# Performance work log

Measured on AMD Instinct MI355X. Metric: run time of the kernel, lower is better.

## Reference

```python
import jax, jax.numpy as jnp
import numpy as np

D_EMB = 1024
D_HEAD = 64
B = 4
T = 4096


def setup_inputs() -> dict:
    key = jax.random.key(0)
    kx, kk, kq, kv = jax.random.split(key, 4)
    s = 1.0 / np.sqrt(D_EMB)  # torch Linear default init scale (uniform bound)
    x = jax.random.normal(kx, (B, T, D_EMB), dtype=jnp.float32)
    Wk = jax.random.uniform(kk, (D_HEAD, D_EMB), jnp.float32, -s, s)
    Wq = jax.random.uniform(kq, (D_HEAD, D_EMB), jnp.float32, -s, s)
    Wv = jax.random.uniform(kv, (D_HEAD, D_EMB), jnp.float32, -s, s)
    return {"x": x, "Wk": Wk, "Wq": Wq, "Wv": Wv}


def reference(x, Wk, Wq, Wv):
    # x: (B, T, d_emb); W*: (d_head, d_emb) -- torch Linear stores (out, in)
    k = jnp.einsum('bte,he->bth', x, Wk)
    q = jnp.einsum('bte,he->bth', x, Wq)
    v = jnp.einsum('bte,he->bth', x, Wv)
    scale = D_HEAD ** (-0.5)
    a = jnp.einsum('bth,bsh->bts', q, k) * scale  # (B, T, T)
    Tlen = x.shape[-2]
    causal = jnp.tril(jnp.ones((Tlen, Tlen), dtype=bool))
    a = jnp.where(causal, a, -jnp.inf)
    a = jax.nn.softmax(a, axis=-1)
    return jnp.einsum('bts,bsh->bth', a, v)  # (B, T, d_head)
```

## Files before the change

### kernel.cpp

```cpp
#include <hip/hip_runtime.h>
#include <hip/hip_bf16.h>

#define D_EMB 1024
#define T_LEN 4096
#define NTASK2 544

typedef short short8 __attribute__((ext_vector_type(8)));
typedef float f32x4 __attribute__((ext_vector_type(4)));
typedef float f32x16 __attribute__((ext_vector_type(16)));
typedef float float4v __attribute__((ext_vector_type(4)));

__device__ __forceinline__ unsigned short f32_to_bf16(float f) {
    union { float f; unsigned int u; } c; c.f = f;
    unsigned int u = c.u;
    return (unsigned short)((u + 0x7FFFu + ((u >> 16) & 1u)) >> 16);
}
__device__ __forceinline__ float bf16_to_f32(unsigned short v) {
    union { unsigned int u; float f; } c; c.u = ((unsigned int)v) << 16;
    return c.f;
}
__device__ __forceinline__ unsigned cvtpk_bf16(float a, float b) {
    unsigned r;
    asm("v_cvt_pk_bf16_f32 %0, %1, %2" : "=v"(r) : "v"(a), "v"(b));
    return r;
}
__device__ __forceinline__ float xhalf_add(float x) {
    return x + __shfl_xor(x, 32);
}
__device__ __forceinline__ void gl_lds16(const void* g, void* l) {
    __builtin_amdgcn_global_load_lds(
        (const __attribute__((address_space(1))) unsigned int*)(g),
        (__attribute__((address_space(3))) unsigned int*)(l), 16, 0, 0);
}

#define QSCALE (0.125f * 1.44269504f)

__global__ __launch_bounds__(256) void convert_w(const float* __restrict__ Wk,
                                                 const float* __restrict__ Wq,
                                                 const float* __restrict__ Wv,
                                                 unsigned short* __restrict__ Wb) {
    int e = (blockIdx.x * 256 + threadIdx.x) * 8;
    const float* src;
    if (e < 65536) src = Wk + e;
    else if (e < 131072) src = Wq + (e - 65536);
    else src = Wv + (e - 131072);
    float4v a0 = *(const float4v*)src;
    float4v a1 = *(const float4v*)(src + 4);
    short8 r;
    r[0] = (short)f32_to_bf16(a0[0]); r[1] = (short)f32_to_bf16(a0[1]);
    r[2] = (short)f32_to_bf16(a0[2]); r[3] = (short)f32_to_bf16(a0[3]);
    r[4] = (short)f32_to_bf16(a1[0]); r[5] = (short)f32_to_bf16(a1[1]);
    r[6] = (short)f32_to_bf16(a1[2]); r[7] = (short)f32_to_bf16(a1[3]);
    int row = e >> 10;
    int dst = e ^ ((row & 7) << 3);
    *(short8*)(Wb + dst) = r;
}

__global__ __launch_bounds__(512) void qkv_chunk(const float* __restrict__ x,
                                                 const unsigned short* __restrict__ Wb,
                                                 unsigned short* __restrict__ Cp) {
    __shared__ __attribute__((aligned(16))) unsigned short Wc[192 * 256];

    int tid = threadIdx.x;
    int lane = tid & 63, wave = tid >> 6;
    int lo = lane & 15, hi = lane >> 4;
    int kc = blockIdx.y;
    int row0 = blockIdx.x * 256;

#pragma unroll
    for (int j = 0; j < 12; j++) {
        int unit = wave * 12 + j;
        int r = unit * 2 + (lane >> 5);
        int cs = lane & 31;
        gl_lds16(Wb + (size_t)r * D_EMB + kc * 256 + cs * 8, &Wc[unit * 512]);
    }
    __syncthreads();

    int xorm = (lo & 7) << 4;
    const char* wbase = (const char*)Wc;

    for (int strip = 0; strip < 2; strip++) {
        int r0 = row0 + wave * 32 + strip * 16;
        const float* xp = x + (size_t)(r0 + lo) * D_EMB + kc * 256 + hi * 8;

        float4v xv[16];
#pragma unroll
        for (int kt = 0; kt < 8; kt++) {
            xv[2 * kt]     = *(const float4v*)(xp + kt * 32);
            xv[2 * kt + 1] = *(const float4v*)(xp + kt * 32 + 4);
        }

        f32x4 acc[12];
#pragma unroll
        for (int i = 0; i < 12; i++) acc[i] = (f32x4){0.f, 0.f, 0.f, 0.f};

#pragma unroll
        for (int kt = 0; kt < 8; kt++) {
            union { unsigned u[4]; short8 s; } c;
            c.u[0] = cvtpk_bf16(xv[2 * kt][0], xv[2 * kt][1]);
            c.u[1] = cvtpk_bf16(xv[2 * kt][2], xv[2 * kt][3]);
            c.u[2] = cvtpk_bf16(xv[2 * kt + 1][0], xv[2 * kt + 1][1]);
            c.u[3] = cvtpk_bf16(xv[2 * kt + 1][2], xv[2 * kt + 1][3]);
            short8 af = c.s;
            int boff = (kt * 64 + hi * 16) ^ xorm;
#pragma unroll
            for (int i = 0; i < 12; i++) {
                short8 bf = *(const short8*)(wbase + (i * 16 + lo) * 512 + boff);
                acc[i] = __builtin_amdgcn_mfma_f32_16x16x32_bf16(af, bf, acc[i], 0, 0, 0);
            }
        }

        size_t cbase = (size_t)kc * 16384 * 192;
#pragma unroll
        for (int i = 0; i < 12; i++) {
#pragma unroll
            for (int rr = 0; rr < 4; rr++) {
                int grow = r0 + hi * 4 + rr;
                Cp[cbase + (size_t)grow * 192 + i * 16 + lo] = f32_to_bf16(acc[i][rr]);
            }
        }
    }
}

__global__ __launch_bounds__(256) void qkv_merge(const unsigned short* __restrict__ Cp,
                                                 unsigned short* __restrict__ Kb,
                                                 unsigned short* __restrict__ Qb,
                                                 unsigned short* __restrict__ Vt) {
    __shared__ unsigned short Vtile[64][72];
    int tid = threadIdx.x;
    int r = tid >> 2, cq = tid & 3;
    int grow = blockIdx.x * 64 + r;

    float s[48];
#pragma unroll
    for (int e = 0; e < 48; e++) s[e] = 0.f;
#pragma unroll
    for (int kc = 0; kc < 4; kc++) {
        const unsigned short* p = Cp + ((size_t)kc * 16384 + grow) * 192 + cq * 48;
#pragma unroll
        for (int g = 0; g < 6; g++) {
            short8 v = *(const short8*)(p + g * 8);
#pragma unroll
            for (int e = 0; e < 8; e++) s[g * 8 + e] += bf16_to_f32((unsigned short)v[e]);
        }
    }
#pragma unroll
    for (int g = 0; g < 6; g++) {
        int col0 = cq * 48 + g * 8;
        if (col0 < 64) {
            short8 v;
#pragma unroll
            for (int e = 0; e < 8; e++) v[e] = (short)f32_to_bf16(s[g * 8 + e]);
            *(short8*)(Kb + (size_t)grow * 64 + col0) = v;
        } else if (col0 < 128) {
            short8 v;
#pragma unroll
            for (int e = 0; e < 8; e++) v[e] = (short)f32_to_bf16(s[g * 8 + e] * QSCALE);
            *(short8*)(Qb + (size_t)grow * 64 + (col0 - 64)) = v;
        } else {
#pragma unroll
            for (int e = 0; e < 8; e++) Vtile[col0 - 128 + e][r] = f32_to_bf16(s[g * 8 + e]);
        }
    }
    __syncthreads();
    int h = tid >> 2, seg = tid & 3;
    int bb = (blockIdx.x * 64) >> 12;
    int t0 = (blockIdx.x * 64) & 4095;
    short8 o0, o1;
#pragma unroll
    for (int e = 0; e < 8; e++) {
        o0[e] = (short)Vtile[h][seg * 16 + e];
        o1[e] = (short)Vtile[h][seg * 16 + 8 + e];
    }
    unsigned short* vd = Vt + ((size_t)bb * 64 + h) * T_LEN + t0 + seg * 16;
    *(short8*)vd = o0;
    *(short8*)(vd + 8) = o1;
}

__global__ __launch_bounds__(64, 3) void attn(const unsigned short* __restrict__ Qb,
                                              const unsigned short* __restrict__ Kb,
                                              const unsigned short* __restrict__ Vt,
                                              unsigned short* __restrict__ Opart,
                                              float* __restrict__ Lpart) {
    int lane = threadIdx.x;
    int q32 = lane & 31;
    int hi = lane >> 5;
    unsigned lin = blockIdx.x;
    int b = lin & 3;
    int s = (int)(((lin >> 3) << 1) | ((lin >> 2) & 1));

    int k = 16, rem = s;
    while (rem >= 4 * k) { rem -= 4 * k; k--; }
    int ti = rem / k;
    int st = 4 * k - 1 - ti;
    int c = rem - ti * k;

    int u0 = c * 8;
    int u1 = min(u0 + 8, 2 * st + 2);
    int ta = 2 * st, tb = ta + 1;
    int qrowA = 64 * st + q32;
    int qrowB = qrowA + 32;

    size_t base = (size_t)b * T_LEN;

    short8 qfa[4], qfb[4];
    const unsigned short* qpa = Qb + (base + qrowA) * 64 + hi * 8;
    const unsigned short* qpb = Qb + (base + qrowB) * 64 + hi * 8;
#pragma unroll
    for (int d = 0; d < 4; d++) {
        qfa[d] = *(const short8*)(qpa + d * 16);
        qfb[d] = *(const short8*)(qpb + d * 16);
    }

    size_t vbase = ((size_t)b * 64 + q32) * T_LEN;
    f32x16 oA0 = {0.f}, oA1 = {0.f}, oB0 = {0.f}, oB1 = {0.f};
    float lA = 0.f, lB = 0.f;

    for (int u = u0; u < u1; ++u) {
        const unsigned short* kp = Kb + (base + u * 32 + q32) * 64 + hi * 8;
        short8 kc0 = *(const short8*)kp;
        short8 kc1 = *(const short8*)(kp + 16);
        short8 kc2 = *(const short8*)(kp + 32);
        short8 kc3 = *(const short8*)(kp + 48);
        const unsigned short* vp = Vt + vbase + u * 32 + hi * 8;
        short8 vc0 = *(const short8*)vp;
        short8 vc1 = *(const short8*)(vp + 16);
        short8 vc2 = *(const short8*)(vp + 32 * T_LEN);
        short8 vc3 = *(const short8*)(vp + 32 * T_LEN + 16);

        f32x16 sa = {0.f}, sb = {0.f};
        sa = __builtin_amdgcn_mfma_f32_32x32x16_bf16(kc0, qfa[0], sa, 0, 0, 0);
        sb = __builtin_amdgcn_mfma_f32_32x32x16_bf16(kc0, qfb[0], sb, 0, 0, 0);
        sa = __builtin_amdgcn_mfma_f32_32x32x16_bf16(kc1, qfa[1], sa, 0, 0, 0);
        sb = __builtin_amdgcn_mfma_f32_32x32x16_bf16(kc1, qfb[1], sb, 0, 0, 0);
        sa = __builtin_amdgcn_mfma_f32_32x32x16_bf16(kc2, qfa[2], sa, 0, 0, 0);
        sb = __builtin_amdgcn_mfma_f32_32x32x16_bf16(kc2, qfb[2], sb, 0, 0, 0);
        sa = __builtin_amdgcn_mfma_f32_32x32x16_bf16(kc3, qfa[3], sa, 0, 0, 0);
        sb = __builtin_amdgcn_mfma_f32_32x32x16_bf16(kc3, qfb[3], sb, 0, 0, 0);

        if (u >= ta) {
#pragma unroll
            for (int r = 0; r < 16; ++r) {
                int key = 32 * u + (r & 3) + 8 * (r >> 2) + 4 * hi;
                sa[r] = (key <= qrowA) ? sa[r] : -3e38f;
                if (u == tb) sb[r] = (key <= qrowB) ? sb[r] : -3e38f;
            }
        }

#pragma unroll
        for (int r = 0; r < 16; ++r) {
            sa[r] = exp2f(sa[r]);
            sb[r] = exp2f(sb[r]);
        }
        float yA = ((sa[0] + sa[8]) + (sa[4] + sa[12])) + ((sa[1] + sa[9]) + (sa[5] + sa[13]))
                 + ((sa[2] + sa[10]) + (sa[6] + sa[14])) + ((sa[3] + sa[11]) + (sa[7] + sa[15]));
        float yB = ((sb[0] + sb[8]) + (sb[4] + sb[12])) + ((sb[1] + sb[9]) + (sb[5] + sb[13]))
                 + ((sb[2] + sb[10]) + (sb[6] + sb[14])) + ((sb[3] + sb[11]) + (sb[7] + sb[15]));
        lA += xhalf_add(yA);
        lB += xhalf_add(yB);

        unsigned pa0 = cvtpk_bf16(sa[0],  sa[1]);
        unsigned pa1 = cvtpk_bf16(sa[2],  sa[3]);
        unsigned pa2 = cvtpk_bf16(sa[4],  sa[5]);
        unsigned pa3 = cvtpk_bf16(sa[6],  sa[7]);
        unsigned pa4 = cvtpk_bf16(sa[8],  sa[9]);
        unsigned pa5 = cvtpk_bf16(sa[10], sa[11]);
        unsigned pa6 = cvtpk_bf16(sa[12], sa[13]);
        unsigned pa7 = cvtpk_bf16(sa[14], sa[15]);
        unsigned pb0 = cvtpk_bf16(sb[0],  sb[1]);
        unsigned pb1 = cvtpk_bf16(sb[2],  sb[3]);
        unsigned pb2 = cvtpk_bf16(sb[4],  sb[5]);
        unsigned pb3 = cvtpk_bf16(sb[6],  sb[7]);
        unsigned pb4 = cvtpk_bf16(sb[8],  sb[9]);
        unsigned pb5 = cvtpk_bf16(sb[10], sb[11]);
        unsigned pb6 = cvtpk_bf16(sb[12], sb[13]);
        unsigned pb7 = cvtpk_bf16(sb[14], sb[15]);
        asm("v_permlane32_swap_b32 %0, %1" : "+v"(pa0), "+v"(pa2));
        asm("v_permlane32_swap_b32 %0, %1" : "+v"(pa1), "+v"(pa3));
        asm("v_permlane32_swap_b32 %0, %1" : "+v"(pa4), "+v"(pa6));
        asm("v_permlane32_swap_b32 %0, %1" : "+v"(pa5), "+v"(pa7));
        asm("v_permlane32_swap_b32 %0, %1" : "+v"(pb0), "+v"(pb2));
        asm("v_permlane32_swap_b32 %0, %1" : "+v"(pb1), "+v"(pb3));
        asm("v_permlane32_swap_b32 %0, %1" : "+v"(pb4), "+v"(pb6));
        asm("v_permlane32_swap_b32 %0, %1" : "+v"(pb5), "+v"(pb7));
        union U8 { unsigned u[4]; short8 s; };
        U8 fA0; fA0.u[0] = pa0; fA0.u[1] = pa1; fA0.u[2] = pa2; fA0.u[3] = pa3;
        U8 fA1; fA1.u[0] = pa4; fA1.u[1] = pa5; fA1.u[2] = pa6; fA1.u[3] = pa7;
        U8 fB0; fB0.u[0] = pb0; fB0.u[1] = pb1; fB0.u[2] = pb2; fB0.u[3] = pb3;
        U8 fB1; fB1.u[0] = pb4; fB1.u[1] = pb5; fB1.u[2] = pb6; fB1.u[3] = pb7;

        oA0 = __builtin_amdgcn_mfma_f32_32x32x16_bf16(vc0, fA0.s, oA0, 0, 0, 0);
        oB0 = __builtin_amdgcn_mfma_f32_32x32x16_bf16(vc0, fB0.s, oB0, 0, 0, 0);
        oA0 = __builtin_amdgcn_mfma_f32_32x32x16_bf16(vc1, fA1.s, oA0, 0, 0, 0);
        oB0 = __builtin_amdgcn_mfma_f32_32x32x16_bf16(vc1, fB1.s, oB0, 0, 0, 0);
        oA1 = __builtin_amdgcn_mfma_f32_32x32x16_bf16(vc2, fA0.s, oA1, 0, 0, 0);
        oB1 = __builtin_amdgcn_mfma_f32_32x32x16_bf16(vc2, fB0.s, oB1, 0, 0, 0);
        oA1 = __builtin_amdgcn_mfma_f32_32x32x16_bf16(vc3, fA1.s, oA1, 0, 0, 0);
        oB1 = __builtin_amdgcn_mfma_f32_32x32x16_bf16(vc3, fB1.s, oB1, 0, 0, 0);
    }

    int slotA = (b * NTASK2 + s) * 2;
    size_t tbA = ((size_t)slotA * 32 + q32) * 64;
    size_t tbB = ((size_t)(slotA + 1) * 32 + q32) * 64;
#pragma unroll
    for (int hb = 0; hb < 2; hb++) {
#pragma unroll
        for (int g = 0; g < 4; g++) {
            float eA0 = hb ? oA1[4 * g] : oA0[4 * g];
            float eA1 = hb ? oA1[4 * g + 1] : oA0[4 * g + 1];
            float eA2 = hb ? oA1[4 * g + 2] : oA0[4 * g + 2];
            float eA3 = hb ? oA1[4 * g + 3] : oA0[4 * g + 3];
            float eB0 = hb ? oB1[4 * g] : oB0[4 * g];
            float eB1 = hb ? oB1[4 * g + 1] : oB0[4 * g + 1];
            float eB2 = hb ? oB1[4 * g + 2] : oB0[4 * g + 2];
            float eB3 = hb ? oB1[4 * g + 3] : oB0[4 * g + 3];
            int h0 = hb * 32 + g * 8 + hi * 4;
            *reinterpret_cast<uint2*>(Opart + tbA + h0) =
                make_uint2(cvtpk_bf16(eA0, eA1), cvtpk_bf16(eA2, eA3));
            *reinterpret_cast<uint2*>(Opart + tbB + h0) =
                make_uint2(cvtpk_bf16(eB0, eB1), cvtpk_bf16(eB2, eB3));
        }
    }
    if (lane < 32) {
        Lpart[slotA * 32 + q32] = lA;
        Lpart[(slotA + 1) * 32 + q32] = lB;
    }
}

__global__ __launch_bounds__(256) void attn_merge(const unsigned short* __restrict__ Opart,
                                                  const float* __restrict__ Lpart,
                                                  float* __restrict__ out) {
    int tid = threadIdx.x;
    int g = blockIdx.x * 64 + (tid >> 2);
    int h0 = (tid & 3) * 16;
    int b = g >> 12, t = g & 4095;
    int tile32 = t >> 5, r32 = t & 31;
    int st = tile32 >> 1, member = tile32 & 1;
    int k = (st >> 2) + 1;
    int sbase = 4 * (136 - ((k * (k + 1)) >> 1));
    int ti = 4 * k - 1 - st;
    int s0 = sbase + ti * k;
    int slot0 = (b * NTASK2 + s0) * 2 + member;

    float ll = 0.f;
    float acc[16];
#pragma unroll
    for (int e = 0; e < 16; e++) acc[e] = 0.f;
    for (int i = 0; i < k; i++) {
        int slot = slot0 + 2 * i;
        ll += Lpart[slot * 32 + r32];
        const unsigned short* op = Opart + ((size_t)slot * 32 + r32) * 64 + h0;
        short8 v0 = *(const short8*)op;
        short8 v1 = *(const short8*)(op + 8);
#pragma unroll
        for (int e = 0; e < 8; e++) {
            acc[e]     += bf16_to_f32((unsigned short)v0[e]);
            acc[8 + e] += bf16_to_f32((unsigned short)v1[e]);
        }
    }
    float inv = 1.f / ll;
    float* dst = out + (size_t)g * 64 + h0;
#pragma unroll
    for (int e = 0; e < 16; e++) dst[e] = acc[e] * inv;
}

extern "C" void kernel_launch(void* const* d_in, const int* in_sizes, int n_in,
                              void* d_out, int out_size, void* d_ws, size_t ws_size,
                              hipStream_t stream) {
    (void)in_sizes; (void)n_in; (void)out_size; (void)ws_size;
    const float* x  = (const float*)d_in[0];
    const float* Wk = (const float*)d_in[1];
    const float* Wq = (const float*)d_in[2];
    const float* Wv = (const float*)d_in[3];
    float* out = (float*)d_out;

    unsigned short* Wb = (unsigned short*)d_ws;
    unsigned short* Kb = Wb + 196608;
    unsigned short* Qb = Kb + 1048576;
    unsigned short* Vt = Qb + 1048576;
    unsigned short* scratch = Vt + 1048576;
    unsigned short* Cp = scratch;
    unsigned short* Opart = scratch;
    float* Lpart = (float*)(scratch + 12582912);

    hipLaunchKernelGGL(convert_w, dim3(96), dim3(256), 0, stream, Wk, Wq, Wv, Wb);
    hipLaunchKernelGGL(qkv_chunk, dim3(64, 4), dim3(512), 0, stream, x, Wb, Cp);
    hipLaunchKernelGGL(qkv_merge, dim3(256), dim3(256), 0, stream, Cp, Kb, Qb, Vt);
    hipLaunchKernelGGL(attn, dim3(4 * NTASK2), dim3(64), 0, stream, Qb, Kb, Vt, Opart, Lpart);
    hipLaunchKernelGGL(attn_merge, dim3(256), dim3(256), 0, stream, Opart, Lpart, out);
}
```

Measured before the change: 75.73 us.

## Split attention work per 32-row query tile and process two key blocks per step

The attention kernel used to give each wave a pair of 32-row query tiles that shared K/V loads. Now each wave owns one 32-row query tile and handles two key blocks per loop iteration. This doubles the task count (1088 per batch) and changes the chunk layout, so the merge kernel's slot indexing is rewritten to match. The goal is a finer split of work and better balance across CUs. The cost is that each K/V load now feeds only one query tile, so K/V traffic per unit of work roughly doubles. The cross-half row-sum reduction also moves out of the loop to run once at the end.

```diff
diff --git a/kernel.cpp b/kernel.cpp
--- a/kernel.cpp
+++ b/kernel.cpp
@@ -3,7 +3,7 @@
 
 #define D_EMB 1024
 #define T_LEN 4096
-#define NTASK2 544
+#define NTASK 1088
 
 typedef short short8 __attribute__((ext_vector_type(8)));
 typedef float f32x4 __attribute__((ext_vector_type(4)));
@@ -189,34 +189,29 @@
     int b = lin & 3;
     int s = (int)(((lin >> 3) << 1) | ((lin >> 2) & 1));
 
-    int k = 16, rem = s;
-    while (rem >= 4 * k) { rem -= 4 * k; k--; }
-    int ti = rem / k;
-    int st = 4 * k - 1 - ti;
-    int c = rem - ti * k;
+    int k = 15, rem = s;
+    while (rem >= 8 * (k + 1)) { rem -= 8 * (k + 1); k--; }
+    int cpt = k + 1;
+    int ti = rem / cpt;
+    int t = (k << 3) + 7 - ti;
+    int c = rem - ti * cpt;
 
     int u0 = c * 8;
-    int u1 = min(u0 + 8, 2 * st + 2);
-    int ta = 2 * st, tb = ta + 1;
-    int qrowA = 64 * st + q32;
-    int qrowB = qrowA + 32;
-
+    int u1 = min(u0 + 8, t + 1);
+    int qrow = t * 32 + q32;
     size_t base = (size_t)b * T_LEN;
 
-    short8 qfa[4], qfb[4];
-    const unsigned short* qpa = Qb + (base + qrowA) * 64 + hi * 8;
-    const unsigned short* qpb = Qb + (base + qrowB) * 64 + hi * 8;
-#pragma unroll
-    for (int d = 0; d < 4; d++) {
-        qfa[d] = *(const short8*)(qpa + d * 16);
-        qfb[d] = *(const short8*)(qpb + d * 16);
-    }
+    short8 qf[4];
+    const unsigned short* qp = Qb + (base + qrow) * 64 + hi * 8;
+#pragma unroll
+    for (int d = 0; d < 4; d++) qf[d] = *(const short8*)(qp + d * 16);
 
     size_t vbase = ((size_t)b * 64 + q32) * T_LEN;
-    f32x16 oA0 = {0.f}, oA1 = {0.f}, oB0 = {0.f}, oB1 = {0.f};
-    float lA = 0.f, lB = 0.f;
-
-    for (int u = u0; u < u1; ++u) {
+    f32x16 o0 = {0.f}, o1 = {0.f};
+    float lacc = 0.f;
+
+    for (int u = u0; u < u1; u += 2) {
+        bool has2 = (u + 1 < u1);
         const unsigned short* kp = Kb + (base + u * 32 + q32) * 64 + hi * 8;
         short8 kc0 = *(const short8*)kp;
         short8 kc1 = *(const short8*)(kp + 16);
@@ -227,37 +222,57 @@
         short8 vc1 = *(const short8*)(vp + 16);
         short8 vc2 = *(const short8*)(vp + 32 * T_LEN);
         short8 vc3 = *(const short8*)(vp + 32 * T_LEN + 16);
+        short8 kd0, kd1, kd2, kd3, vd0, vd1, vd2, vd3;
+        if (has2) {
+            const unsigned short* kp2 = kp + 32 * 64;
+            kd0 = *(const short8*)kp2;
+            kd1 = *(const short8*)(kp2 + 16);
+            kd2 = *(const short8*)(kp2 + 32);
+            kd3 = *(const short8*)(kp2 + 48);
+            const unsigned short* vp2 = vp + 32;
+            vd0 = *(const short8*)vp2;
+            vd1 = *(const short8*)(vp2 + 16);
+            vd2 = *(const short8*)(vp2 + 32 * T_LEN);
+            vd3 = *(const short8*)(vp2 + 32 * T_LEN + 16);
+        }
 
         f32x16 sa = {0.f}, sb = {0.f};
-        sa = __builtin_amdgcn_mfma_f32_32x32x16_bf16(kc0, qfa[0], sa, 0, 0, 0);
-        sb = __builtin_amdgcn_mfma_f32_32x32x16_bf16(kc0, qfb[0], sb, 0, 0, 0);
-        sa = __builtin_amdgcn_mfma_f32_32x32x16_bf16(kc1, qfa[1], sa, 0, 0, 0);
-        sb = __builtin_amdgcn_mfma_f32_32x32x16_bf16(kc1, qfb[1], sb, 0, 0, 0);
-        sa = __builtin_amdgcn_mfma_f32_32x32x16_bf16(kc2, qfa[2], sa, 0, 0, 0);
-        sb = __builtin_amdgcn_mfma_f32_32x32x16_bf16(kc2, qfb[2], sb, 0, 0, 0);
-        sa = __builtin_amdgcn_mfma_f32_32x32x16_bf16(kc3, qfa[3], sa, 0, 0, 0);
-        sb = __builtin_amdgcn_mfma_f32_32x32x16_bf16(kc3, qfb[3], sb, 0, 0, 0);
-
-        if (u >= ta) {
+        sa = __builtin_amdgcn_mfma_f32_32x32x16_bf16(kc0, qf[0], sa, 0, 0, 0);
+        if (has2) sb = __builtin_amdgcn_mfma_f32_32x32x16_bf16(kd0, qf[0], sb, 0, 0, 0);
+        sa = __builtin_amdgcn_mfma_f32_32x32x16_bf16(kc1, qf[1], sa, 0, 0, 0);
+        if (has2) sb = __builtin_amdgcn_mfma_f32_32x32x16_bf16(kd1, qf[1], sb, 0, 0, 0);
+        sa = __builtin_amdgcn_mfma_f32_32x32x16_bf16(kc2, qf[2], sa, 0, 0, 0);
+        if (has2) sb = __builtin_amdgcn_mfma_f32_32x32x16_bf16(kd2, qf[2], sb, 0, 0, 0);
+        sa = __builtin_amdgcn_mfma_f32_32x32x16_bf16(kc3, qf[3], sa, 0, 0, 0);
+        if (has2) sb = __builtin_amdgcn_mfma_f32_32x32x16_bf16(kd3, qf[3], sb, 0, 0, 0);
+
+        if (u == t) {
 #pragma unroll
             for (int r = 0; r < 16; ++r) {
                 int key = 32 * u + (r & 3) + 8 * (r >> 2) + 4 * hi;
-                sa[r] = (key <= qrowA) ? sa[r] : -3e38f;
-                if (u == tb) sb[r] = (key <= qrowB) ? sb[r] : -3e38f;
+                sa[r] = (key <= qrow) ? sa[r] : -3e38f;
             }
         }
-
-#pragma unroll
-        for (int r = 0; r < 16; ++r) {
-            sa[r] = exp2f(sa[r]);
-            sb[r] = exp2f(sb[r]);
-        }
+        if (has2 && u + 1 == t) {
+#pragma unroll
+            for (int r = 0; r < 16; ++r) {
+                int key = 32 * (u + 1) + (r & 3) + 8 * (r >> 2) + 4 * hi;
+                sb[r] = (key <= qrow) ? sb[r] : -3e38f;
+            }
+        }
+
+#pragma unroll
+        for (int r = 0; r < 16; ++r) sa[r] = exp2f(sa[r]);
         float yA = ((sa[0] + sa[8]) + (sa[4] + sa[12])) + ((sa[1] + sa[9]) + (sa[5] + sa[13]))
                  + ((sa[2] + sa[10]) + (sa[6] + sa[14])) + ((sa[3] + sa[11]) + (sa[7] + sa[15]));
-        float yB = ((sb[0] + sb[8]) + (sb[4] + sb[12])) + ((sb[1] + sb[9]) + (sb[5] + sb[13]))
-                 + ((sb[2] + sb[10]) + (sb[6] + sb[14])) + ((sb[3] + sb[11]) + (sb[7] + sb[15]));
-        lA += xhalf_add(yA);
-        lB += xhalf_add(yB);
+        lacc += yA;
+        if (has2) {
+#pragma unroll
+            for (int r = 0; r < 16; ++r) sb[r] = exp2f(sb[r]);
+            float yB = ((sb[0] + sb[8]) + (sb[4] + sb[12])) + ((sb[1] + sb[9]) + (sb[5] + sb[13]))
+                     + ((sb[2] + sb[10]) + (sb[6] + sb[14])) + ((sb[3] + sb[11]) + (sb[7] + sb[15]));
+            lacc += yB;
+        }
 
         unsigned pa0 = cvtpk_bf16(sa[0],  sa[1]);
         unsigned pa1 = cvtpk_bf16(sa[2],  sa[3]);
@@ -267,63 +282,59 @@
         unsigned pa5 = cvtpk_bf16(sa[10], sa[11]);
         unsigned pa6 = cvtpk_bf16(sa[12], sa[13]);
         unsigned pa7 = cvtpk_bf16(sa[14], sa[15]);
-        unsigned pb0 = cvtpk_bf16(sb[0],  sb[1]);
-        unsigned pb1 = cvtpk_bf16(sb[2],  sb[3]);
-        unsigned pb2 = cvtpk_bf16(sb[4],  sb[5]);
-        unsigned pb3 = cvtpk_bf16(sb[6],  sb[7]);
-        unsigned pb4 = cvtpk_bf16(sb[8],  sb[9]);
-        unsigned pb5 = cvtpk_bf16(sb[10], sb[11]);
-        unsigned pb6 = cvtpk_bf16(sb[12], sb[13]);
-        unsigned pb7 = cvtpk_bf16(sb[14], sb[15]);
         asm("v_permlane32_swap_b32 %0, %1" : "+v"(pa0), "+v"(pa2));
         asm("v_permlane32_swap_b32 %0, %1" : "+v"(pa1), "+v"(pa3));
         asm("v_permlane32_swap_b32 %0, %1" : "+v"(pa4), "+v"(pa6));
         asm("v_permlane32_swap_b32 %0, %1" : "+v"(pa5), "+v"(pa7));
-        asm("v_permlane32_swap_b32 %0, %1" : "+v"(pb0), "+v"(pb2));
-        asm("v_permlane32_swap_b32 %0, %1" : "+v"(pb1), "+v"(pb3));
-        asm("v_permlane32_swap_b32 %0, %1" : "+v"(pb4), "+v"(pb6));
-        asm("v_permlane32_swap_b32 %0, %1" : "+v"(pb5), "+v"(pb7));
         union U8 { unsigned u[4]; short8 s; };
         U8 fA0; fA0.u[0] = pa0; fA0.u[1] = pa1; fA0.u[2] = pa2; fA0.u[3] = pa3;
         U8 fA1; fA1.u[0] = pa4; fA1.u[1] = pa5; fA1.u[2] = pa6; fA1.u[3] = pa7;
-        U8 fB0; fB0.u[0] = pb0; fB0.u[1] = pb1; fB0.u[2] = pb2; fB0.u[3] = pb3;
-        U8 fB1; fB1.u[0] = pb4; fB1.u[1] = pb5; fB1.u[2] = pb6; fB1.u[3] = pb7;
-
-        oA0 = __builtin_amdgcn_mfma_f32_32x32x16_bf16(vc0, fA0.s, oA0, 0, 0, 0);
-        oB0 = __builtin_amdgcn_mfma_f32_32x32x16_bf16(vc0, fB0.s, oB0, 0, 0, 0);
-        oA0 = __builtin_amdgcn_mfma_f32_32x32x16_bf16(vc1, fA1.s, oA0, 0, 0, 0);
-        oB0 = __builtin_amdgcn_mfma_f32_32x32x16_bf16(vc1, fB1.s, oB0, 0, 0, 0);
-        oA1 = __builtin_amdgcn_mfma_f32_32x32x16_bf16(vc2, fA0.s, oA1, 0, 0, 0);
-        oB1 = __builtin_amdgcn_mfma_f32_32x32x16_bf16(vc2, fB0.s, oB1, 0, 0, 0);
-        oA1 = __builtin_amdgcn_mfma_f32_32x32x16_bf16(vc3, fA1.s, oA1, 0, 0, 0);
-        oB1 = __builtin_amdgcn_mfma_f32_32x32x16_bf16(vc3, fB1.s, oB1, 0, 0, 0);
-    }
-
-    int slotA = (b * NTASK2 + s) * 2;
-    size_t tbA = ((size_t)slotA * 32 + q32) * 64;
-    size_t tbB = ((size_t)(slotA + 1) * 32 + q32) * 64;
+        o0 = __builtin_amdgcn_mfma_f32_32x32x16_bf16(vc0, fA0.s, o0, 0, 0, 0);
+        o0 = __builtin_amdgcn_mfma_f32_32x32x16_bf16(vc1, fA1.s, o0, 0, 0, 0);
+        o1 = __builtin_amdgcn_mfma_f32_32x32x16_bf16(vc2, fA0.s, o1, 0, 0, 0);
+        o1 = __builtin_amdgcn_mfma_f32_32x32x16_bf16(vc3, fA1.s, o1, 0, 0, 0);
+
+        if (has2) {
+            unsigned pb0 = cvtpk_bf16(sb[0],  sb[1]);
+            unsigned pb1 = cvtpk_bf16(sb[2],  sb[3]);
+            unsigned pb2 = cvtpk_bf16(sb[4],  sb[5]);
+            unsigned pb3 = cvtpk_bf16(sb[6],  sb[7]);
+            unsigned pb4 = cvtpk_bf16(sb[8],  sb[9]);
+            unsigned pb5 = cvtpk_bf16(sb[10], sb[11]);
+            unsigned pb6 = cvtpk_bf16(sb[12], sb[13]);
+            unsigned pb7 = cvtpk_bf16(sb[14], sb[15]);
+            asm("v_permlane32_swap_b32 %0, %1" : "+v"(pb0), "+v"(pb2));
+            asm("v_permlane32_swap_b32 %0, %1" : "+v"(pb1), "+v"(pb3));
+            asm("v_permlane32_swap_b32 %0, %1" : "+v"(pb4), "+v"(pb6));
+            asm("v_permlane32_swap_b32 %0, %1" : "+v"(pb5), "+v"(pb7));
+            U8 fB0; fB0.u[0] = pb0; fB0.u[1] = pb1; fB0.u[2] = pb2; fB0.u[3] = pb3;
+            U8 fB1; fB1.u[0] = pb4; fB1.u[1] = pb5; fB1.u[2] = pb6; fB1.u[3] = pb7;
+            o0 = __builtin_amdgcn_mfma_f32_32x32x16_bf16(vd0, fB0.s, o0, 0, 0, 0);
+            o0 = __builtin_amdgcn_mfma_f32_32x32x16_bf16(vd1, fB1.s, o0, 0, 0, 0);
+            o1 = __builtin_amdgcn_mfma_f32_32x32x16_bf16(vd2, fB0.s, o1, 0, 0, 0);
+            o1 = __builtin_amdgcn_mfma_f32_32x32x16_bf16(vd3, fB1.s, o1, 0, 0, 0);
+        }
+    }
+
+    lacc = xhalf_add(lacc);
+
+    int slot = b * NTASK + s;
+    size_t tbase = ((size_t)slot * 32 + q32) * 64;
 #pragma unroll
     for (int hb = 0; hb < 2; hb++) {
 #pragma unroll
         for (int g = 0; g < 4; g++) {
-            float eA0 = hb ? oA1[4 * g] : oA0[4 * g];
-            float eA1 = hb ? oA1[4 * g + 1] : oA0[4 * g + 1];
-            float eA2 = hb ? oA1[4 * g + 2] : oA0[4 * g + 2];
-            float eA3 = hb ? oA1[4 * g + 3] : oA0[4 * g + 3];
-            float eB0 = hb ? oB1[4 * g] : oB0[4 * g];
-            float eB1 = hb ? oB1[4 * g + 1] : oB0[4 * g + 1];
-            float eB2 = hb ? oB1[4 * g + 2] : oB0[4 * g + 2];
-            float eB3 = hb ? oB1[4 * g + 3] : oB0[4 * g + 3];
+            float e0 = hb ? o1[4 * g] : o0[4 * g];
+            float e1 = hb ? o1[4 * g + 1] : o0[4 * g + 1];
+            float e2 = hb ? o1[4 * g + 2] : o0[4 * g + 2];
+            float e3 = hb ? o1[4 * g + 3] : o0[4 * g + 3];
             int h0 = hb * 32 + g * 8 + hi * 4;
-            *reinterpret_cast<uint2*>(Opart + tbA + h0) =
-                make_uint2(cvtpk_bf16(eA0, eA1), cvtpk_bf16(eA2, eA3));
-            *reinterpret_cast<uint2*>(Opart + tbB + h0) =
-                make_uint2(cvtpk_bf16(eB0, eB1), cvtpk_bf16(eB2, eB3));
+            *reinterpret_cast<uint2*>(Opart + tbase + h0) =
+                make_uint2(cvtpk_bf16(e0, e1), cvtpk_bf16(e2, e3));
         }
     }
     if (lane < 32) {
-        Lpart[slotA * 32 + q32] = lA;
-        Lpart[(slotA + 1) * 32 + q32] = lB;
+        Lpart[slot * 32 + q32] = lacc;
     }
 }
 
@@ -334,20 +345,18 @@
     int g = blockIdx.x * 64 + (tid >> 2);
     int h0 = (tid & 3) * 16;
     int b = g >> 12, t = g & 4095;
-    int tile32 = t >> 5, r32 = t & 31;
-    int st = tile32 >> 1, member = tile32 & 1;
-    int k = (st >> 2) + 1;
-    int sbase = 4 * (136 - ((k * (k + 1)) >> 1));
-    int ti = 4 * k - 1 - st;
-    int s0 = sbase + ti * k;
-    int slot0 = (b * NTASK2 + s0) * 2 + member;
+    int tile = t >> 5, r32 = t & 31;
+    int k = tile >> 3;
+    int nch = k + 1;
+    int s0 = 8 * (136 - (((k + 1) * (k + 2)) >> 1)) + (7 - (tile & 7)) * nch;
+    int tb = b * NTASK + s0;
 
     float ll = 0.f;
     float acc[16];
 #pragma unroll
     for (int e = 0; e < 16; e++) acc[e] = 0.f;
-    for (int i = 0; i < k; i++) {
-        int slot = slot0 + 2 * i;
+    for (int i = 0; i < nch; i++) {
+        int slot = tb + i;
         ll += Lpart[slot * 32 + r32];
         const unsigned short* op = Opart + ((size_t)slot * 32 + r32) * 64 + h0;
         short8 v0 = *(const short8*)op;
@@ -386,6 +395,6 @@
     hipLaunchKernelGGL(convert_w, dim3(96), dim3(256), 0, stream, Wk, Wq, Wv, Wb);
     hipLaunchKernelGGL(qkv_chunk, dim3(64, 4), dim3(512), 0, stream, x, Wb, Cp);
     hipLaunchKernelGGL(qkv_merge, dim3(256), dim3(256), 0, stream, Cp, Kb, Qb, Vt);
-    hipLaunchKernelGGL(attn, dim3(4 * NTASK2), dim3(64), 0, stream, Qb, Kb, Vt, Opart, Lpart);
+    hipLaunchKernelGGL(attn, dim3(4 * NTASK), dim3(64), 0, stream, Qb, Kb, Vt, Opart, Lpart);
     hipLaunchKernelGGL(attn_merge, dim3(256), dim3(256), 0, stream, Opart, Lpart, out);
 }
```

Result: slower. 85.11 us (+12.4%).

## Split attention key loop across two wavefronts with LDS reduction

Applied to the files above, without the earlier changes.

The attention kernel now launches 128 threads per block, and the two wavefronts each process alternating key tiles of the same query chunk. The second wave writes its partial output accumulators and row sums to shared memory, and the first wave adds them in before writing Opart/Lpart. This doubles the wavefronts available to hide latency on the short per-task loops, at the cost of an LDS reduction, a block barrier, and one idle wave during the epilogue.

```diff
diff --git a/kernel.cpp b/kernel.cpp
--- a/kernel.cpp
+++ b/kernel.cpp
@@ -177,12 +177,16 @@
     *(short8*)(vd + 8) = o1;
 }
 
-__global__ __launch_bounds__(64, 3) void attn(const unsigned short* __restrict__ Qb,
-                                              const unsigned short* __restrict__ Kb,
-                                              const unsigned short* __restrict__ Vt,
-                                              unsigned short* __restrict__ Opart,
-                                              float* __restrict__ Lpart) {
-    int lane = threadIdx.x;
+__global__ __launch_bounds__(128, 3) void attn(const unsigned short* __restrict__ Qb,
+                                               const unsigned short* __restrict__ Kb,
+                                               const unsigned short* __restrict__ Vt,
+                                               unsigned short* __restrict__ Opart,
+                                               float* __restrict__ Lpart) {
+    __shared__ float Osh[64][65];
+    __shared__ float Lsh[64][2];
+
+    int tid = threadIdx.x;
+    int lane = tid & 63, wv = tid >> 6;
     int q32 = lane & 31;
     int hi = lane >> 5;
     unsigned lin = blockIdx.x;
@@ -216,7 +220,7 @@
     f32x16 oA0 = {0.f}, oA1 = {0.f}, oB0 = {0.f}, oB1 = {0.f};
     float lA = 0.f, lB = 0.f;
 
-    for (int u = u0; u < u1; ++u) {
+    for (int u = u0 + wv; u < u1; u += 2) {
         const unsigned short* kp = Kb + (base + u * 32 + q32) * 64 + hi * 8;
         short8 kc0 = *(const short8*)kp;
         short8 kc1 = *(const short8*)(kp + 16);
@@ -256,8 +260,8 @@
                  + ((sa[2] + sa[10]) + (sa[6] + sa[14])) + ((sa[3] + sa[11]) + (sa[7] + sa[15]));
         float yB = ((sb[0] + sb[8]) + (sb[4] + sb[12])) + ((sb[1] + sb[9]) + (sb[5] + sb[13]))
                  + ((sb[2] + sb[10]) + (sb[6] + sb[14])) + ((sb[3] + sb[11]) + (sb[7] + sb[15]));
-        lA += xhalf_add(yA);
-        lB += xhalf_add(yB);
+        lA += yA;
+        lB += yB;
 
         unsigned pa0 = cvtpk_bf16(sa[0],  sa[1]);
         unsigned pa1 = cvtpk_bf16(sa[2],  sa[3]);
@@ -299,31 +303,55 @@
         oB1 = __builtin_amdgcn_mfma_f32_32x32x16_bf16(vc3, fB1.s, oB1, 0, 0, 0);
     }
 
-    int slotA = (b * NTASK2 + s) * 2;
-    size_t tbA = ((size_t)slotA * 32 + q32) * 64;
-    size_t tbB = ((size_t)(slotA + 1) * 32 + q32) * 64;
-#pragma unroll
-    for (int hb = 0; hb < 2; hb++) {
-#pragma unroll
-        for (int g = 0; g < 4; g++) {
-            float eA0 = hb ? oA1[4 * g] : oA0[4 * g];
-            float eA1 = hb ? oA1[4 * g + 1] : oA0[4 * g + 1];
-            float eA2 = hb ? oA1[4 * g + 2] : oA0[4 * g + 2];
-            float eA3 = hb ? oA1[4 * g + 3] : oA0[4 * g + 3];
-            float eB0 = hb ? oB1[4 * g] : oB0[4 * g];
-            float eB1 = hb ? oB1[4 * g + 1] : oB0[4 * g + 1];
-            float eB2 = hb ? oB1[4 * g + 2] : oB0[4 * g + 2];
-            float eB3 = hb ? oB1[4 * g + 3] : oB0[4 * g + 3];
-            int h0 = hb * 32 + g * 8 + hi * 4;
-            *reinterpret_cast<uint2*>(Opart + tbA + h0) =
-                make_uint2(cvtpk_bf16(eA0, eA1), cvtpk_bf16(eA2, eA3));
-            *reinterpret_cast<uint2*>(Opart + tbB + h0) =
-                make_uint2(cvtpk_bf16(eB0, eB1), cvtpk_bf16(eB2, eB3));
-        }
-    }
-    if (lane < 32) {
-        Lpart[slotA * 32 + q32] = lA;
-        Lpart[(slotA + 1) * 32 + q32] = lB;
+    if (wv == 1) {
+#pragma unroll
+        for (int r = 0; r < 16; ++r) {
+            Osh[lane][r]      = oA0[r];
+            Osh[lane][16 + r] = oA1[r];
+            Osh[lane][32 + r] = oB0[r];
+            Osh[lane][48 + r] = oB1[r];
+        }
+        Lsh[lane][0] = lA;
+        Lsh[lane][1] = lB;
+    }
+    __syncthreads();
+    if (wv == 0) {
+#pragma unroll
+        for (int r = 0; r < 16; ++r) {
+            oA0[r] += Osh[lane][r];
+            oA1[r] += Osh[lane][16 + r];
+            oB0[r] += Osh[lane][32 + r];
+            oB1[r] += Osh[lane][48 + r];
+        }
+        lA = xhalf_add(lA + Lsh[lane][0]);
+        lB = xhalf_add(lB + Lsh[lane][1]);
+
+        int slotA = (b * NTASK2 + s) * 2;
+        size_t tbA = ((size_t)slotA * 32 + q32) * 64;
+        size_t tbB = ((size_t)(slotA + 1) * 32 + q32) * 64;
+#pragma unroll
+        for (int hb = 0; hb < 2; hb++) {
+#pragma unroll
+            for (int g = 0; g < 4; g++) {
+                float eA0 = hb ? oA1[4 * g] : oA0[4 * g];
+                float eA1 = hb ? oA1[4 * g + 1] : oA0[4 * g + 1];
+                float eA2 = hb ? oA1[4 * g + 2] : oA0[4 * g + 2];
+                float eA3 = hb ? oA1[4 * g + 3] : oA0[4 * g + 3];
+                float eB0 = hb ? oB1[4 * g] : oB0[4 * g];
+                float eB1 = hb ? oB1[4 * g + 1] : oB0[4 * g + 1];
+                float eB2 = hb ? oB1[4 * g + 2] : oB0[4 * g + 2];
+                float eB3 = hb ? oB1[4 * g + 3] : oB0[4 * g + 3];
+                int h0 = hb * 32 + g * 8 + hi * 4;
+                *reinterpret_cast<uint2*>(Opart + tbA + h0) =
+                    make_uint2(cvtpk_bf16(eA0, eA1), cvtpk_bf16(eA2, eA3));
+                *reinterpret_cast<uint2*>(Opart + tbB + h0) =
+                    make_uint2(cvtpk_bf16(eB0, eB1), cvtpk_bf16(eB2, eB3));
+            }
+        }
+        if (lane < 32) {
+            Lpart[slotA * 32 + q32] = lA;
+            Lpart[(slotA + 1) * 32 + q32] = lB;
+        }
     }
 }
 
@@ -386,6 +414,6 @@
     hipLaunchKernelGGL(convert_w, dim3(96), dim3(256), 0, stream, Wk, Wq, Wv, Wb);
     hipLaunchKernelGGL(qkv_chunk, dim3(64, 4), dim3(512), 0, stream, x, Wb, Cp);
     hipLaunchKernelGGL(qkv_merge, dim3(256), dim3(256), 0, stream, Cp, Kb, Qb, Vt);
-    hipLaunchKernelGGL(attn, dim3(4 * NTASK2), dim3(64), 0, stream, Qb, Kb, Vt, Opart, Lpart);
+    hipLaunchKernelGGL(attn, dim3(4 * NTASK2), dim3(128), 0, stream, Qb, Kb, Vt, Opart, Lpart);
     hipLaunchKernelGGL(attn_merge, dim3(256), dim3(256), 0, stream, Opart, Lpart, out);
 }
```

New measurement: 78.30 us. 3.4% more time.
